# Kernel tuning notes

Hardware: AMD Instinct MI355X
Metric: run time of the kernel (lower is better)

Reference implementation:

```python
import jax, jax.numpy as jnp
import numpy as np

C_IN = 1024
C_MID = 512  # in_channels // shrink_factor


def conv1x1(x, w, b):
    # x: [B, Cin, H, W], w: [Cout, Cin], b: [Cout]
    return jnp.einsum('bchw,oc->bohw', x, w) + b[None, :, None, None]


def setup_inputs() -> dict:
    key = jax.random.key(0)
    ks = jax.random.split(key, 9)
    B, H, W = 8, 48, 48
    x = jax.random.normal(ks[0], (B, C_IN, H, W), dtype=jnp.float32)
    s = 0.02
    w1 = jax.random.normal(ks[1], (C_MID, C_IN), dtype=jnp.float32) * s
    b1 = jnp.zeros((C_MID,), dtype=jnp.float32)
    w2 = jax.random.normal(ks[2], (C_MID, C_IN), dtype=jnp.float32) * s
    b2 = jnp.zeros((C_MID,), dtype=jnp.float32)
    w3 = jax.random.normal(ks[3], (C_MID, C_IN), dtype=jnp.float32) * s
    b3 = jnp.zeros((C_MID,), dtype=jnp.float32)
    w4 = jax.random.normal(ks[4], (C_IN, C_MID), dtype=jnp.float32) * s
    b4 = jnp.zeros((C_IN,), dtype=jnp.float32)
    return {'x': x, 'w1': w1, 'b1': b1, 'w2': w2, 'b2': b2,
            'w3': w3, 'b3': b3, 'w4': w4, 'b4': b4}


def reference(x, w1, b1, w2, b2, w3, b3, w4, b4):
    B, C, H, W = x.shape
    # 1x1 conv projections (theta, phi, g), each [B, C_MID, H, W]
    x_theta = conv1x1(x, w1, b1)
    x_phi = conv1x1(x, w2, b2)
    x_g = conv1x1(x, w3, b3)
    # NOTE: the original uses raw .view() (no transpose); torch and jnp are both
    # row-major, so jnp.reshape reproduces the exact same memory reinterpretation.
    x_g = x_g.reshape(B, -1, C_MID)      # [B, N, C_MID]
    x_theta = x_theta.reshape(B, -1, C_MID)  # [B, N, C_MID]
    x_phi = x_phi.reshape(B, C_MID, -1)  # [B, C_MID, N]
    # full dense N x N affinity (N = H*W)
    att = jnp.einsum('bnc,bcm->bnm', x_theta, x_phi)
    att = jax.nn.softmax(att, axis=-1)
    y = jnp.einsum('bnm,bmc->bnc', att, x_g)  # [B, N, C_MID]
    y = y.reshape(B, C_MID, H, W)
    x_last = conv1x1(y, w4, b4)  # [B, C_IN, H, W]
    return x + x_last
```

## Files before the change

kernel.cpp:

```cpp
#include <hip/hip_runtime.h>

typedef unsigned short u16;
typedef __bf16 bf16x8_t __attribute__((ext_vector_type(8)));
typedef float f32x4_t __attribute__((ext_vector_type(4)));

__device__ __forceinline__ u16 f2bf(float f) {
  unsigned u = __builtin_bit_cast(unsigned, f);
  u += 0x7FFFu + ((u >> 16) & 1u);
  return (u16)(u >> 16);
}
__device__ __forceinline__ float bf2f(u16 h) {
  unsigned u = ((unsigned)h) << 16;
  return __builtin_bit_cast(float, u);
}

typedef __attribute__((address_space(1))) const unsigned gas_u32;
typedef __attribute__((address_space(3))) unsigned las_u32;
__device__ __forceinline__ void gload16(const void* g, void* l) {
  __builtin_amdgcn_global_load_lds((gas_u32*)g, (las_u32*)l, 16, 0, 0);
}

#define SBAR()                                  \
  do {                                          \
    __builtin_amdgcn_sched_barrier(0);          \
    asm volatile("" ::: "memory");              \
    __builtin_amdgcn_s_barrier();               \
    asm volatile("" ::: "memory");              \
    __builtin_amdgcn_sched_barrier(0);          \
  } while (0)
#define VM4() asm volatile("s_waitcnt vmcnt(4)" ::: "memory")

__global__ __launch_bounds__(256) void cast4_kernel(
    const float* __restrict__ a0, const float* __restrict__ a1,
    const float* __restrict__ a2, const float* __restrict__ a3,
    u16* __restrict__ out) {
  const int z = blockIdx.z;
  const float* a = (z == 0) ? a0 : (z == 1) ? a1 : (z == 2) ? a2 : a3;
  const int i = blockIdx.x * 256 + threadIdx.x;
  out[(size_t)z * 524288 + i] = f2bf(a[i]);
}

__global__ __launch_bounds__(256) void bcat_kernel(
    const float* __restrict__ b1, const float* __restrict__ b3,
    float* __restrict__ o) {
  const int i = blockIdx.x * 256 + threadIdx.x;
  o[i] = (i < 512) ? b1[i] : b3[i - 512];
}

__global__ __launch_bounds__(256) void cast_transpose_kernel(
    const float* __restrict__ in, u16* __restrict__ out, int R, int C,
    long sIn, long sOut) {
  __shared__ u16 t[32][33];
  const int b = blockIdx.z;
  in += (long)b * sIn;
  out += (long)b * sOut;
  const int c0 = blockIdx.x * 32, r0 = blockIdx.y * 32;
  const int tx = threadIdx.x, ty = threadIdx.y;
#pragma unroll
  for (int i = 0; i < 32; i += 8)
    t[ty + i][tx] = f2bf(in[(long)(r0 + ty + i) * C + c0 + tx]);
  __syncthreads();
#pragma unroll
  for (int i = 0; i < 32; i += 8)
    out[(long)(c0 + ty + i) * R + r0 + tx] = t[tx][ty + i];
}

__global__ __launch_bounds__(256) void transpose64(
    const u16* __restrict__ in, u16* __restrict__ out, int R, int C, long sIn,
    long sOut) {
  __shared__ u16 t[64][66];
  const int b = blockIdx.z;
  in += (long)b * sIn;
  out += (long)b * sOut;
  const int c0 = blockIdx.x * 64, r0 = blockIdx.y * 64;
  const int tx = threadIdx.x & 31, ty = threadIdx.x >> 5;
#pragma unroll
  for (int i = 0; i < 64; i += 8) {
    unsigned v = *(const unsigned*)&in[(long)(r0 + ty + i) * C + c0 + 2 * tx];
    t[ty + i][2 * tx] = (u16)v;
    t[ty + i][2 * tx + 1] = (u16)(v >> 16);
  }
  __syncthreads();
#pragma unroll
  for (int i = 0; i < 64; i += 8) {
    unsigned lo = t[2 * tx][ty + i], hi = t[2 * tx + 1][ty + i];
    *(unsigned*)&out[(long)(c0 + ty + i) * R + r0 + 2 * tx] = lo | (hi << 16);
  }
}

#define STG_A(bufv, h, kt)                                          \
  do {                                                              \
    const char* g_ = Ag + (size_t)(kt) * 128 + (size_t)(h)*AH;      \
    char* d_ = sAd + (bufv)*32768 + (h)*16384;                      \
    gload16(g_, d_);                                                \
    gload16(g_ + AC, d_ + 8192);                                    \
  } while (0)
#define STG_B(bufv, h, kt)                                          \
  do {                                                              \
    const char* g_ = Bg + (size_t)(kt) * 128 + (size_t)(h)*BH;      \
    char* d_ = sBd + (bufv)*32768 + (h)*16384;                      \
    gload16(g_, d_);                                                \
    gload16(g_ + BC, d_ + 8192);                                    \
  } while (0)
#define LOAD_A(bufv, mh)                                                     \
  _Pragma("unroll") for (int m = 0; m < 4; m++) {                            \
    const int lr_ = (mh)*128 + wr * 64 + m * 16 + l15;                       \
    af[m][0] = *(const bf16x8_t*)(lds + (bufv)*32768 + lr_ * 128 + koff0);   \
    af[m][1] =                                                               \
        *(const bf16x8_t*)(lds + (bufv)*32768 + lr_ * 128 + (koff0 ^ 64));   \
  }
#define LOAD_B(bufv, nh)                                                     \
  _Pragma("unroll") for (int n = 0; n < 2; n++) {                            \
    const int lr_ = (nh)*128 + wc * 32 + n * 16 + l15;                       \
    bfr[(nh)*2 + n][0] =                                                     \
        *(const bf16x8_t*)(lds + 65536 + (bufv)*32768 + lr_ * 128 + koff0);  \
    bfr[(nh)*2 + n][1] = *(const bf16x8_t*)(lds + 65536 + (bufv)*32768 +     \
                                            lr_ * 128 + (koff0 ^ 64));       \
  }
#define MMA(mh, nh)                                                          \
  __builtin_amdgcn_s_setprio(1);                                            \
  _Pragma("unroll") for (int m = 0; m < 4; m++)                              \
      _Pragma("unroll") for (int n = 0; n < 2; n++)                          \
          _Pragma("unroll") for (int kk = 0; kk < 2; kk++)                   \
              acc[(mh)*4 + m][(nh)*2 + n] =                                  \
      __builtin_amdgcn_mfma_f32_16x16x32_bf16(                               \
          af[m][kk], bfr[(nh)*2 + n][kk], acc[(mh)*4 + m][(nh)*2 + n], 0, 0, \
          0);                                                                \
  __builtin_amdgcn_s_setprio(0);

template <int MODE>
__global__ __launch_bounds__(512, 2) void gemm8(
    const u16* __restrict__ A, const u16* __restrict__ B,
    void* __restrict__ C0, void* __restrict__ C1, void* __restrict__ C2,
    const u16* __restrict__ W2, const float* __restrict__ bias,
    const float* __restrict__ bias2, const float* __restrict__ resid,
    float* __restrict__ stats) {
  constexpr int LDA_ = (MODE == 0) ? 1024 : (MODE == 3) ? 2304 : 512;
  constexpr int LDB_ = (MODE == 0) ? 1024 : (MODE == 3) ? 2304 : 512;
  constexpr int KK = (MODE == 0) ? 1024 : (MODE == 3) ? 2304 : 512;
  constexpr int NT = KK >> 6;
  constexpr size_t AH = 64ull * LDA_ * 2, AC = 128ull * LDA_ * 2;
  constexpr size_t BH = 32ull * LDB_ * 2, BC = 128ull * LDB_ * 2;

  __shared__ alignas(16) char lds[131072];
  const int tid = threadIdx.x;
  const int w = tid >> 6, l = tid & 63;
  const int wr = w >> 2, wc = w & 3;
  const int l15 = l & 15, lhi = l >> 4;
  const int koff0 = (lhi * 16) ^ ((l & 7) << 4);

  unsigned bx, by, bz;
  bool roleB = false;
  if constexpr (MODE == 0) {
    unsigned bid = blockIdx.x;
    unsigned swz = (bid & 7u) * 54u + (bid >> 3);
    roleB = (swz >= 288u);
    unsigned s = roleB ? swz - 288u : swz;
    if (roleB) { bx = s % 2u; by = (s / 2u) % 9u; bz = s / 18u; }
    else       { bx = s % 9u; by = (s / 9u) % 4u; bz = s / 36u; }
  } else {
    const unsigned gx = gridDim.x, gy = gridDim.y;
    const unsigned nb = gx * gy * gridDim.z;
    unsigned bid = blockIdx.x + gx * (blockIdx.y + gy * blockIdx.z);
    bid = (bid & 7u) * (nb >> 3) + (bid >> 3);
    bx = bid % gx;
    unsigned t1 = bid / gx;
    by = t1 % gy;
    bz = t1 / gy;
  }
  const int rowbase = by * 256, colbase = bx * 256;

  const u16* Abase;
  const u16* Bbase;
  if constexpr (MODE == 0) {
    Abase = roleB ? (B + (size_t)bz * 2359296) : A;
    Bbase = roleB ? W2 : (B + (size_t)bz * 2359296);
  } else if constexpr (MODE == 1) {
    Abase = A + (size_t)bz * 1179648;
    Bbase = B + (size_t)bz * 1179648;
  } else if constexpr (MODE == 3) {
    Abase = A + (size_t)bz * 5308416;
    Bbase = B + (size_t)bz * 1179648;
  } else {
    Abase = A;
    Bbase = B + (size_t)bz * 1179648;
  }

  const int sub = tid >> 3;
  const int kb = ((tid & 7) * 16) ^ ((sub & 7) << 4);
  const char* Ag = (const char*)(Abase + (size_t)(rowbase + sub) * LDA_) + kb;
  const char* Bg =
      (const char*)(Bbase + (size_t)(colbase + (sub >> 5) * 64 + (sub & 31)) *
                                LDB_) +
      kb;
  char* sAd = lds + w * 1024;
  char* sBd = lds + 65536 + w * 1024;

  f32x4_t acc[8][4] = {};
  bf16x8_t af[4][2], bfr[4][2];

  STG_A(0, 0, 0); STG_B(0, 0, 0);
  STG_A(0, 1, 0); STG_B(0, 1, 0);
  STG_A(1, 0, 1); STG_B(1, 0, 1);
  VM4();
  SBAR();

  for (int t = 0; t < NT; ++t) {
    const int c = t & 1;
    const int tn = (t + 1 < NT) ? t + 1 : NT - 1;
    const int tn2 = (t + 2 < NT) ? t + 2 : NT - 1;
    LOAD_A(c, 0);
    LOAD_B(c, 0);
    STG_A(c ^ 1, 1, tn);
    SBAR();
    MMA(0, 0);
    SBAR();
    LOAD_B(c, 1);
    STG_B(c ^ 1, 1, tn);
    SBAR();
    MMA(0, 1);
    SBAR();
    LOAD_A(c, 1);
    STG_A(c, 0, tn2);
    SBAR();
    MMA(1, 0);
    SBAR();
    STG_B(c, 0, tn2);
    VM4();
    SBAR();
    MMA(1, 1);
    SBAR();
  }

  if constexpr (MODE == 0) {
    if (!roleB) {
      const int rb = rowbase + wr * 128;
      const int which = rb >> 9;
      u16* Cp = (u16*)(which ? C1 : C0) + (size_t)bz * 1179648;
      const int rowout0 = rb - which * 512;
#pragma unroll
      for (int mf = 0; mf < 8; mf++)
#pragma unroll
        for (int r = 0; r < 4; r++) {
          const int ro = mf * 16 + lhi * 4 + r;
          const float bv = bias[rb + ro];
          const size_t rowo = (size_t)(rowout0 + ro) * 2304;
#pragma unroll
          for (int nf = 0; nf < 4; nf++) {
            const int col = colbase + wc * 64 + nf * 16 + l15;
            Cp[rowo + col] = f2bf(acc[mf][nf][r] + bv);
          }
        }
    } else {
      u16* Cp = (u16*)C2 + (size_t)bz * 1179648;
#pragma unroll
      for (int mf = 0; mf < 8; mf++)
#pragma unroll
        for (int r = 0; r < 4; r++) {
          const size_t rowo =
              (size_t)(rowbase + wr * 128 + mf * 16 + lhi * 4 + r) * 512;
#pragma unroll
          for (int nf = 0; nf < 4; nf++) {
            const int col = colbase + wc * 64 + nf * 16 + l15;
            Cp[rowo + col] = f2bf(acc[mf][nf][r] + bias2[col]);
          }
        }
    }
  } else if constexpr (MODE == 1) {
    u16* Cp = (u16*)C0 + (size_t)bz * 5308416;
#pragma unroll
    for (int mf = 0; mf < 8; mf++)
#pragma unroll
      for (int r = 0; r < 4; r++) {
        const int row = rowbase + wr * 128 + mf * 16 + lhi * 4 + r;
        float sm = 0.f;
#pragma unroll
        for (int nf = 0; nf < 4; nf++) {
          const int col = colbase + wc * 64 + nf * 16 + l15;
          const u16 hb = f2bf(__expf(acc[mf][nf][r]));
          Cp[(size_t)row * 2304 + col] = hb;
          sm += bf2f(hb);
        }
#pragma unroll
        for (int mk = 1; mk < 16; mk <<= 1) sm += __shfl_xor(sm, mk);
        if (l15 == 0)
          stats[((size_t)bz * 36 + bx * 4 + wc) * 2304 + row] = sm;
      }
  } else if constexpr (MODE == 3) {
    u16* Cp = (u16*)C0 + (size_t)bz * 1179648;
#pragma unroll
    for (int mf = 0; mf < 8; mf++)
#pragma unroll
      for (int r = 0; r < 4; r++) {
        const int row = rowbase + wr * 128 + mf * 16 + lhi * 4 + r;
        const float invs = stats[(size_t)bz * 2304 + row];
#pragma unroll
        for (int nf = 0; nf < 4; nf++) {
          const int col = colbase + wc * 64 + nf * 16 + l15;
          Cp[(size_t)row * 512 + col] = f2bf(acc[mf][nf][r] * invs);
        }
      }
  } else {
    float* Cp = (float*)C0 + (size_t)bz * 2359296;
    const float* rp = resid + (size_t)bz * 2359296;
#pragma unroll
    for (int mf = 0; mf < 8; mf++)
#pragma unroll
      for (int r = 0; r < 4; r++) {
        const int row = rowbase + wr * 128 + mf * 16 + lhi * 4 + r;
        const float bv = bias[row];
#pragma unroll
        for (int nf = 0; nf < 4; nf++) {
          const int col = colbase + wc * 64 + nf * 16 + l15;
          Cp[(size_t)row * 2304 + col] =
              acc[mf][nf][r] + bv + rp[(size_t)row * 2304 + col];
        }
      }
  }
}

__global__ __launch_bounds__(256) void reduce_sums(
    const float* __restrict__ stats, float* __restrict__ rowinv) {
  const int i = blockIdx.x * 256 + threadIdx.x;
  const int bz = i / 2304, n = i % 2304;
  const float* s = stats + (size_t)bz * 36 * 2304 + n;
  float S = 0.f;
  for (int j = 0; j < 36; j++) S += s[(size_t)j * 2304];
  rowinv[i] = 1.0f / S;
}

extern "C" void kernel_launch(void* const* d_in, const int* in_sizes, int n_in,
                              void* d_out, int out_size, void* d_ws,
                              size_t ws_size, hipStream_t stream) {
  const float* x = (const float*)d_in[0];
  const float* w1 = (const float*)d_in[1];
  const float* b1 = (const float*)d_in[2];
  const float* w2 = (const float*)d_in[3];
  const float* b2 = (const float*)d_in[4];
  const float* w3 = (const float*)d_in[5];
  const float* b3 = (const float*)d_in[6];
  const float* w4 = (const float*)d_in[7];
  const float* b4 = (const float*)d_in[8];
  float* out = (float*)d_out;
  char* ws = (char*)d_ws;

  if (ws_size < 268435456ull) return;
  u16* p_xT = (u16*)(ws);
  u16* p_gn = (u16*)(ws + 37748736);
  float* p_bcat = (float*)(ws + 56623104);
  u16* p_att = (u16*)(ws);
  float* p_stats = (float*)(ws + 84934656);
  float* p_rinv = (float*)(ws + 87588864);
  u16* p_wb = (u16*)(ws + 169869312);
  u16* p_theta = (u16*)(ws + 174063616);
  u16* p_phiT = (u16*)(ws + 192937984);
  u16* p_gT = (u16*)(ws + 211812352);
  u16* p_y = (u16*)(ws + 230686720);
  u16* p_yrT = (u16*)(ws + 249561088);

  cast4_kernel<<<dim3(2048, 1, 4), 256, 0, stream>>>(w1, w3, w2, w4, p_wb);
  bcat_kernel<<<dim3(4), 256, 0, stream>>>(b1, b3, p_bcat);
  cast_transpose_kernel<<<dim3(72, 32, 8), dim3(32, 8), 0, stream>>>(
      x, p_xT, 1024, 2304, 2359296L, 2359296L);
  gemm8<0><<<dim3(432), 512, 0, stream>>>(
      p_wb, p_xT, p_theta, p_gn, p_phiT, p_wb + 1048576, p_bcat, b2, nullptr,
      nullptr);
  transpose64<<<dim3(8, 36, 8), 256, 0, stream>>>(p_gn, p_gT, 2304, 512,
                                                  1179648L, 1179648L);
  gemm8<1><<<dim3(9, 9, 8), 512, 0, stream>>>(
      p_theta, p_phiT, p_att, nullptr, nullptr, nullptr, nullptr, nullptr,
      nullptr, p_stats);
  reduce_sums<<<dim3(72), 256, 0, stream>>>(p_stats, p_rinv);
  gemm8<3><<<dim3(2, 9, 8), 512, 0, stream>>>(
      p_att, p_gT, p_y, nullptr, nullptr, nullptr, nullptr, nullptr, nullptr,
      p_rinv);
  transpose64<<<dim3(36, 8, 8), 256, 0, stream>>>(p_y, p_yrT, 512, 2304,
                                                  1179648L, 1179648L);
  gemm8<2><<<dim3(9, 4, 8), 512, 0, stream>>>(
      p_wb + 1572864, p_yrT, out, nullptr, nullptr, nullptr, b4, nullptr, x,
      nullptr);
}
```

Measured before the change: 308.7 us.

## Fuse attention score, exp, and PV GEMMs into one flash-style kernel

```diff
diff --git a/kernel.cpp b/kernel.cpp
--- a/kernel.cpp
+++ b/kernel.cpp
@@ -28,7 +28,11 @@
     asm volatile("" ::: "memory");              \
     __builtin_amdgcn_sched_barrier(0);          \
   } while (0)
+#define VM0() asm volatile("s_waitcnt vmcnt(0)" ::: "memory")
+#define VM2() asm volatile("s_waitcnt vmcnt(2)" ::: "memory")
 #define VM4() asm volatile("s_waitcnt vmcnt(4)" ::: "memory")
+#define VM8() asm volatile("s_waitcnt vmcnt(8)" ::: "memory")
+#define LGKM0() asm volatile("s_waitcnt lgkmcnt(0)" ::: "memory")
 
 __global__ __launch_bounds__(256) void cast4_kernel(
     const float* __restrict__ a0, const float* __restrict__ a1,
@@ -133,11 +137,10 @@
     const u16* __restrict__ A, const u16* __restrict__ B,
     void* __restrict__ C0, void* __restrict__ C1, void* __restrict__ C2,
     const u16* __restrict__ W2, const float* __restrict__ bias,
-    const float* __restrict__ bias2, const float* __restrict__ resid,
-    float* __restrict__ stats) {
-  constexpr int LDA_ = (MODE == 0) ? 1024 : (MODE == 3) ? 2304 : 512;
-  constexpr int LDB_ = (MODE == 0) ? 1024 : (MODE == 3) ? 2304 : 512;
-  constexpr int KK = (MODE == 0) ? 1024 : (MODE == 3) ? 2304 : 512;
+    const float* __restrict__ bias2, const float* __restrict__ resid) {
+  constexpr int LDA_ = (MODE == 0) ? 1024 : 512;
+  constexpr int LDB_ = (MODE == 0) ? 1024 : 512;
+  constexpr int KK = (MODE == 0) ? 1024 : 512;
   constexpr int NT = KK >> 6;
   constexpr size_t AH = 64ull * LDA_ * 2, AC = 128ull * LDA_ * 2;
   constexpr size_t BH = 32ull * LDB_ * 2, BC = 128ull * LDB_ * 2;
@@ -175,12 +178,6 @@
   if constexpr (MODE == 0) {
     Abase = roleB ? (B + (size_t)bz * 2359296) : A;
     Bbase = roleB ? W2 : (B + (size_t)bz * 2359296);
-  } else if constexpr (MODE == 1) {
-    Abase = A + (size_t)bz * 1179648;
-    Bbase = B + (size_t)bz * 1179648;
-  } else if constexpr (MODE == 3) {
-    Abase = A + (size_t)bz * 5308416;
-    Bbase = B + (size_t)bz * 1179648;
   } else {
     Abase = A;
     Bbase = B + (size_t)bz * 1179648;
@@ -266,40 +263,6 @@
           }
         }
     }
-  } else if constexpr (MODE == 1) {
-    u16* Cp = (u16*)C0 + (size_t)bz * 5308416;
-#pragma unroll
-    for (int mf = 0; mf < 8; mf++)
-#pragma unroll
-      for (int r = 0; r < 4; r++) {
-        const int row = rowbase + wr * 128 + mf * 16 + lhi * 4 + r;
-        float sm = 0.f;
-#pragma unroll
-        for (int nf = 0; nf < 4; nf++) {
-          const int col = colbase + wc * 64 + nf * 16 + l15;
-          const u16 hb = f2bf(__expf(acc[mf][nf][r]));
-          Cp[(size_t)row * 2304 + col] = hb;
-          sm += bf2f(hb);
-        }
-#pragma unroll
-        for (int mk = 1; mk < 16; mk <<= 1) sm += __shfl_xor(sm, mk);
-        if (l15 == 0)
-          stats[((size_t)bz * 36 + bx * 4 + wc) * 2304 + row] = sm;
-      }
-  } else if constexpr (MODE == 3) {
-    u16* Cp = (u16*)C0 + (size_t)bz * 1179648;
-#pragma unroll
-    for (int mf = 0; mf < 8; mf++)
-#pragma unroll
-      for (int r = 0; r < 4; r++) {
-        const int row = rowbase + wr * 128 + mf * 16 + lhi * 4 + r;
-        const float invs = stats[(size_t)bz * 2304 + row];
-#pragma unroll
-        for (int nf = 0; nf < 4; nf++) {
-          const int col = colbase + wc * 64 + nf * 16 + l15;
-          Cp[(size_t)row * 512 + col] = f2bf(acc[mf][nf][r] * invs);
-        }
-      }
   } else {
     float* Cp = (float*)C0 + (size_t)bz * 2359296;
     const float* rp = resid + (size_t)bz * 2359296;
@@ -319,14 +282,181 @@
   }
 }
 
-__global__ __launch_bounds__(256) void reduce_sums(
-    const float* __restrict__ stats, float* __restrict__ rowinv) {
-  const int i = blockIdx.x * 256 + threadIdx.x;
-  const int bz = i / 2304, n = i % 2304;
-  const float* s = stats + (size_t)bz * 36 * 2304 + n;
-  float S = 0.f;
-  for (int j = 0; j < 36; j++) S += s[(size_t)j * 2304];
-  rowinv[i] = 1.0f / S;
+__global__ __launch_bounds__(512, 1) void fused_attn(
+    const u16* __restrict__ TH, const u16* __restrict__ PHI,
+    const u16* __restrict__ GT, u16* __restrict__ Y) {
+  __shared__ alignas(16) char lds[163840];
+  const int tid = threadIdx.x;
+  const int w = tid >> 6, l = tid & 63;
+  const int l15 = l & 15, lhi = l >> 4;
+  const int koff0 = (lhi * 16) ^ ((l & 7) << 4);
+  const int wr = w >> 2, wcS = w & 3;
+  const int nloc = wcS * 16 + l15;
+
+  unsigned bid = blockIdx.x;
+  bid = (bid & 7u) * 36u + (bid >> 3);
+  const unsigned bz = bid / 36u, iq = bid % 36u;
+  const int n0 = iq * 64;
+
+  const int sub = tid >> 3;
+  const int kb = ((tid & 7) * 16) ^ ((sub & 7) << 4);
+
+  const char* THb =
+      (const char*)(TH + (size_t)bz * 1179648 + (size_t)(n0 + sub) * 512) + kb;
+  const char* PHb0 =
+      (const char*)(PHI + (size_t)bz * 1179648 + (size_t)sub * 512) + kb;
+  const char* GTb0 =
+      (const char*)(GT + (size_t)bz * 1179648 + (size_t)sub * 2304) + kb;
+  u16* Yb = Y + (size_t)bz * 1179648;
+  float* rsf = (float*)(lds + 65536);
+
+  f32x4_t yacc[4][4] = {};
+  float pr = 0.f;
+  bf16x8_t af[4][2], bfr[4][2], bt[2];
+
+#define S_STG_A(bufv, h, kt)                                           \
+  do {                                                                 \
+    const char* g_ = PHm + (size_t)(kt)*128 + (size_t)(h)*65536;       \
+    char* d_ = lds + (bufv)*32768 + (h)*16384 + w * 1024;              \
+    gload16(g_, d_);                                                   \
+    gload16(g_ + 131072, d_ + 8192);                                   \
+  } while (0)
+#define S_STG_T(bufv, kt)                                              \
+  gload16(THb + (size_t)(kt)*128, lds + 65536 + (bufv)*8192 + w * 1024)
+#define S_LOAD_A(bufv, mh)                                                   \
+  _Pragma("unroll") for (int m = 0; m < 4; m++) {                            \
+    const int lr_ = (mh)*128 + wr * 64 + m * 16 + l15;                       \
+    af[m][0] = *(const bf16x8_t*)(lds + (bufv)*32768 + lr_ * 128 + koff0);   \
+    af[m][1] =                                                               \
+        *(const bf16x8_t*)(lds + (bufv)*32768 + lr_ * 128 + (koff0 ^ 64));   \
+  }
+#define S_LOAD_T(bufv)                                                       \
+  do {                                                                       \
+    const int lr_ = wcS * 16 + l15;                                          \
+    bt[0] =                                                                  \
+        *(const bf16x8_t*)(lds + 65536 + (bufv)*8192 + lr_ * 128 + koff0);   \
+    bt[1] = *(const bf16x8_t*)(lds + 65536 + (bufv)*8192 + lr_ * 128 +       \
+                               (koff0 ^ 64));                                \
+  } while (0)
+#define S_MMA(mh)                                                            \
+  __builtin_amdgcn_s_setprio(1);                                            \
+  _Pragma("unroll") for (int m = 0; m < 4; m++)                              \
+      _Pragma("unroll") for (int kk = 0; kk < 2; kk++)                       \
+          sacc[(mh)*4 + m] = __builtin_amdgcn_mfma_f32_16x16x32_bf16(        \
+              af[m][kk], bt[kk], sacc[(mh)*4 + m], 0, 0, 0);                 \
+  __builtin_amdgcn_s_setprio(0);
+#define PV_STG_G(bufv, ks)                                                   \
+  _Pragma("unroll") for (int q = 0; q < 8; q++)                              \
+      gload16(GTm + (size_t)q * 294912 + (size_t)(ks)*128,                   \
+              lds + (bufv)*65536 + q * 8192 + w * 1024);
+#define PV_LOAD_A(ks)                                                        \
+  _Pragma("unroll") for (int m = 0; m < 4; m++) {                            \
+    const int br_ = m * 16 + l15;                                            \
+    af[m][0] = *(const bf16x8_t*)(lds + 131072 + br_ * 512 +                 \
+                                  (((ks)*128 + lhi * 16) ^                   \
+                                   ((l15 & 7) << 4)));                       \
+    af[m][1] = *(const bf16x8_t*)(lds + 131072 + br_ * 512 +                 \
+                                  (((ks)*128 + 64 + lhi * 16) ^              \
+                                   ((l15 & 7) << 4)));                       \
+  }
+#define PV_LOAD_G(bufv)                                                      \
+  _Pragma("unroll") for (int n = 0; n < 4; n++) {                            \
+    const int lr_ = w * 64 + n * 16 + l15;                                   \
+    bfr[n][0] = *(const bf16x8_t*)(lds + (bufv)*65536 + lr_ * 128 + koff0);  \
+    bfr[n][1] =                                                              \
+        *(const bf16x8_t*)(lds + (bufv)*65536 + lr_ * 128 + (koff0 ^ 64));   \
+  }
+#define PV_MMA()                                                             \
+  __builtin_amdgcn_s_setprio(1);                                            \
+  _Pragma("unroll") for (int m = 0; m < 4; m++)                              \
+      _Pragma("unroll") for (int n = 0; n < 4; n++)                          \
+          _Pragma("unroll") for (int kk = 0; kk < 2; kk++)                   \
+              yacc[m][n] = __builtin_amdgcn_mfma_f32_16x16x32_bf16(          \
+                  af[m][kk], bfr[n][kk], yacc[m][n], 0, 0, 0);               \
+  __builtin_amdgcn_s_setprio(0);
+
+  for (int mt = 0; mt < 9; ++mt) {
+    const char* PHm = PHb0 + (size_t)mt * 262144;
+    const char* GTm = GTb0 + (size_t)mt * 512;
+
+    f32x4_t sacc[8] = {};
+    S_STG_A(0, 0, 0); S_STG_A(0, 1, 0); S_STG_T(0, 0);
+    S_STG_A(1, 0, 1);
+    VM2();
+    SBAR();
+    for (int t = 0; t < 8; ++t) {
+      const int c = t & 1;
+      const int tn = (t + 1 < 8) ? t + 1 : 7;
+      const int tn2 = (t + 2 < 8) ? t + 2 : 7;
+      S_LOAD_A(c, 0);
+      S_LOAD_T(c);
+      S_STG_A(c ^ 1, 1, tn);
+      S_STG_T(c ^ 1, tn);
+      SBAR();
+      S_MMA(0);
+      SBAR();
+      S_LOAD_A(c, 1);
+      S_STG_A(c, 0, tn2);
+      SBAR();
+      S_MMA(1);
+      VM2();
+      SBAR();
+    }
+
+#pragma unroll
+    for (int mf = 0; mf < 8; mf++)
+#pragma unroll
+      for (int r = 0; r < 4; r++) {
+        const int mm = wr * 128 + (mf >> 2) * 64 + (mf & 3) * 16 + lhi * 4 + r;
+        const u16 hb = f2bf(__expf(sacc[mf][r]));
+        pr += bf2f(hb);
+        *(u16*)(lds + 131072 + nloc * 512 +
+                ((2 * mm) ^ ((nloc & 7) << 4))) = hb;
+      }
+    VM0();
+    LGKM0();
+    SBAR();
+
+    PV_STG_G(0, 0);
+    for (int ks = 0; ks < 4; ++ks) {
+      const int c = ks & 1;
+      if (ks < 3) {
+        PV_STG_G(c ^ 1, ks + 1);
+        VM8();
+      } else {
+        VM0();
+      }
+      SBAR();
+      PV_LOAD_A(ks);
+      PV_LOAD_G(c);
+      PV_MMA();
+      SBAR();
+    }
+  }
+
+  SBAR();
+  if (tid < 64) rsf[tid] = 0.f;
+  LGKM0();
+  SBAR();
+  float prs = pr;
+  prs += __shfl_xor(prs, 16);
+  prs += __shfl_xor(prs, 32);
+  if (lhi == 0) atomicAdd(&rsf[nloc], prs);
+  LGKM0();
+  SBAR();
+#pragma unroll
+  for (int mf = 0; mf < 4; mf++)
+#pragma unroll
+    for (int r = 0; r < 4; r++) {
+      const int n = mf * 16 + lhi * 4 + r;
+      const float inv = 1.0f / rsf[n];
+      const size_t rowo = (size_t)(n0 + n) * 512;
+#pragma unroll
+      for (int nf = 0; nf < 4; nf++) {
+        const int d = w * 64 + nf * 16 + l15;
+        Yb[rowo + d] = f2bf(yacc[mf][nf][r] * inv);
+      }
+    }
 }
 
 extern "C" void kernel_launch(void* const* d_in, const int* in_sizes, int n_in,
@@ -348,9 +478,6 @@
   u16* p_xT = (u16*)(ws);
   u16* p_gn = (u16*)(ws + 37748736);
   float* p_bcat = (float*)(ws + 56623104);
-  u16* p_att = (u16*)(ws);
-  float* p_stats = (float*)(ws + 84934656);
-  float* p_rinv = (float*)(ws + 87588864);
   u16* p_wb = (u16*)(ws + 169869312);
   u16* p_theta = (u16*)(ws + 174063616);
   u16* p_phiT = (u16*)(ws + 192937984);
@@ -363,20 +490,12 @@
   cast_transpose_kernel<<<dim3(72, 32, 8), dim3(32, 8), 0, stream>>>(
       x, p_xT, 1024, 2304, 2359296L, 2359296L);
   gemm8<0><<<dim3(432), 512, 0, stream>>>(
-      p_wb, p_xT, p_theta, p_gn, p_phiT, p_wb + 1048576, p_bcat, b2, nullptr,
-      nullptr);
+      p_wb, p_xT, p_theta, p_gn, p_phiT, p_wb + 1048576, p_bcat, b2, nullptr);
   transpose64<<<dim3(8, 36, 8), 256, 0, stream>>>(p_gn, p_gT, 2304, 512,
                                                   1179648L, 1179648L);
-  gemm8<1><<<dim3(9, 9, 8), 512, 0, stream>>>(
-      p_theta, p_phiT, p_att, nullptr, nullptr, nullptr, nullptr, nullptr,
-      nullptr, p_stats);
-  reduce_sums<<<dim3(72), 256, 0, stream>>>(p_stats, p_rinv);
-  gemm8<3><<<dim3(2, 9, 8), 512, 0, stream>>>(
-      p_att, p_gT, p_y, nullptr, nullptr, nullptr, nullptr, nullptr, nullptr,
-      p_rinv);
+  fused_attn<<<dim3(288), 512, 0, stream>>>(p_theta, p_phiT, p_gT, p_y);
   transpose64<<<dim3(36, 8, 8), 256, 0, stream>>>(p_y, p_yrT, 512, 2304,
                                                   1179648L, 1179648L);
   gemm8<2><<<dim3(9, 4, 8), 512, 0, stream>>>(
-      p_wb + 1572864, p_yrT, out, nullptr, nullptr, nullptr, b4, nullptr, x,
-      nullptr);
-}
+      p_wb + 1572864, p_yrT, out, nullptr, nullptr, nullptr, b4, nullptr, x);
+}
```

Result: slower. 366.5 us (+18.7%).

## Replace PV GEMM with dedicated 256x128-tile kernel for better CU occupancy

Applied to the files above, without the earlier changes.

```diff
diff --git a/kernel.cpp b/kernel.cpp
--- a/kernel.cpp
+++ b/kernel.cpp
@@ -28,6 +28,7 @@
     asm volatile("" ::: "memory");              \
     __builtin_amdgcn_sched_barrier(0);          \
   } while (0)
+#define VM2() asm volatile("s_waitcnt vmcnt(2)" ::: "memory")
 #define VM4() asm volatile("s_waitcnt vmcnt(4)" ::: "memory")
 
 __global__ __launch_bounds__(256) void cast4_kernel(
@@ -135,9 +136,9 @@
     const u16* __restrict__ W2, const float* __restrict__ bias,
     const float* __restrict__ bias2, const float* __restrict__ resid,
     float* __restrict__ stats) {
-  constexpr int LDA_ = (MODE == 0) ? 1024 : (MODE == 3) ? 2304 : 512;
-  constexpr int LDB_ = (MODE == 0) ? 1024 : (MODE == 3) ? 2304 : 512;
-  constexpr int KK = (MODE == 0) ? 1024 : (MODE == 3) ? 2304 : 512;
+  constexpr int LDA_ = (MODE == 0) ? 1024 : 512;
+  constexpr int LDB_ = (MODE == 0) ? 1024 : 512;
+  constexpr int KK = (MODE == 0) ? 1024 : 512;
   constexpr int NT = KK >> 6;
   constexpr size_t AH = 64ull * LDA_ * 2, AC = 128ull * LDA_ * 2;
   constexpr size_t BH = 32ull * LDB_ * 2, BC = 128ull * LDB_ * 2;
@@ -178,9 +179,6 @@
   } else if constexpr (MODE == 1) {
     Abase = A + (size_t)bz * 1179648;
     Bbase = B + (size_t)bz * 1179648;
-  } else if constexpr (MODE == 3) {
-    Abase = A + (size_t)bz * 5308416;
-    Bbase = B + (size_t)bz * 1179648;
   } else {
     Abase = A;
     Bbase = B + (size_t)bz * 1179648;
@@ -286,20 +284,6 @@
         if (l15 == 0)
           stats[((size_t)bz * 36 + bx * 4 + wc) * 2304 + row] = sm;
       }
-  } else if constexpr (MODE == 3) {
-    u16* Cp = (u16*)C0 + (size_t)bz * 1179648;
-#pragma unroll
-    for (int mf = 0; mf < 8; mf++)
-#pragma unroll
-      for (int r = 0; r < 4; r++) {
-        const int row = rowbase + wr * 128 + mf * 16 + lhi * 4 + r;
-        const float invs = stats[(size_t)bz * 2304 + row];
-#pragma unroll
-        for (int nf = 0; nf < 4; nf++) {
-          const int col = colbase + wc * 64 + nf * 16 + l15;
-          Cp[(size_t)row * 512 + col] = f2bf(acc[mf][nf][r] * invs);
-        }
-      }
   } else {
     float* Cp = (float*)C0 + (size_t)bz * 2359296;
     const float* rp = resid + (size_t)bz * 2359296;
@@ -327,6 +311,120 @@
   float S = 0.f;
   for (int j = 0; j < 36; j++) S += s[(size_t)j * 2304];
   rowinv[i] = 1.0f / S;
+}
+
+__global__ __launch_bounds__(512, 1) void pv128(
+    const u16* __restrict__ A, const u16* __restrict__ B, u16* __restrict__ C,
+    const float* __restrict__ rowinv) {
+  constexpr int NT = 36;
+  constexpr size_t AH = 64ull * 2304 * 2, AC = 128ull * 2304 * 2;
+  constexpr size_t BHp = 64ull * 2304 * 2;
+
+  __shared__ alignas(16) char lds[98304];
+  const int tid = threadIdx.x;
+  const int w = tid >> 6, l = tid & 63;
+  const int wr = w >> 2, wc = w & 3;
+  const int l15 = l & 15, lhi = l >> 4;
+  const int koff0 = (lhi * 16) ^ ((l & 7) << 4);
+
+  const unsigned swz = (blockIdx.x & 7u) * 36u + (blockIdx.x >> 3);
+  const unsigned bz = swz / 36u, rem = swz % 36u;
+  const unsigned by = rem >> 2, bx = rem & 3u;
+  const int rowbase = by * 256, colbase = bx * 128;
+
+  const int sub = tid >> 3;
+  const int kb = ((tid & 7) * 16) ^ ((sub & 7) << 4);
+  const char* Ag =
+      (const char*)(A + (size_t)bz * 5308416 + (size_t)(rowbase + sub) * 2304) +
+      kb;
+  const char* Bg =
+      (const char*)(B + (size_t)bz * 1179648 + (size_t)(colbase + sub) * 2304) +
+      kb;
+  char* sAd = lds + w * 1024;
+
+#define PSTG_A(bufv, h, kt)                                          \
+  do {                                                               \
+    const char* g_ = Ag + (size_t)(kt) * 128 + (size_t)(h)*AH;       \
+    char* d_ = sAd + (bufv)*32768 + (h)*16384;                       \
+    gload16(g_, d_);                                                 \
+    gload16(g_ + AC, d_ + 8192);                                     \
+  } while (0)
+#define PSTG_B(bufv, h, kt)                                          \
+  gload16(Bg + (size_t)(kt) * 128 + (size_t)(h)*BHp,                 \
+          lds + 65536 + (bufv)*16384 + (h)*8192 + w * 1024)
+#define PLOAD_A(bufv, mh)                                                    \
+  _Pragma("unroll") for (int m = 0; m < 4; m++) {                            \
+    const int lr_ = (mh)*128 + wr * 64 + m * 16 + l15;                       \
+    af[m][0] = *(const bf16x8_t*)(lds + (bufv)*32768 + lr_ * 128 + koff0);   \
+    af[m][1] =                                                               \
+        *(const bf16x8_t*)(lds + (bufv)*32768 + lr_ * 128 + (koff0 ^ 64));   \
+  }
+#define PLOAD_B(bufv)                                                        \
+  _Pragma("unroll") for (int n = 0; n < 2; n++) {                            \
+    const int cc_ = wc * 32 + n * 16 + l15;                                  \
+    const int base_ = 65536 + (bufv)*16384 + (wc >> 1) * 8192 +              \
+                      (cc_ & 63) * 128;                                      \
+    bfr[n][0] = *(const bf16x8_t*)(lds + base_ + koff0);                     \
+    bfr[n][1] = *(const bf16x8_t*)(lds + base_ + (koff0 ^ 64));              \
+  }
+#define PMMA(mh)                                                             \
+  __builtin_amdgcn_s_setprio(1);                                            \
+  _Pragma("unroll") for (int m = 0; m < 4; m++)                              \
+      _Pragma("unroll") for (int n = 0; n < 2; n++)                          \
+          _Pragma("unroll") for (int kk = 0; kk < 2; kk++)                   \
+              acc[(mh)*4 + m][n] = __builtin_amdgcn_mfma_f32_16x16x32_bf16(  \
+                  af[m][kk], bfr[n][kk], acc[(mh)*4 + m][n], 0, 0, 0);       \
+  __builtin_amdgcn_s_setprio(0);
+
+  f32x4_t acc[8][2] = {};
+  bf16x8_t af[4][2], bfr[2][2];
+
+  PSTG_A(0, 0, 0);
+  PSTG_A(0, 1, 0);
+  PSTG_B(0, 0, 0);
+  PSTG_B(0, 1, 0);
+  PSTG_A(1, 0, 1);
+  VM2();
+  SBAR();
+
+  for (int t = 0; t < NT; ++t) {
+    const int c = t & 1;
+    const int tn = (t + 1 < NT) ? t + 1 : NT - 1;
+    const int tn2 = (t + 2 < NT) ? t + 2 : NT - 1;
+    PLOAD_A(c, 0);
+    PLOAD_B(c);
+    PSTG_A(c ^ 1, 1, tn);
+    PSTG_B(c ^ 1, 0, tn);
+    PSTG_B(c ^ 1, 1, tn);
+    SBAR();
+    PMMA(0);
+    SBAR();
+    PLOAD_A(c, 1);
+    PSTG_A(c, 0, tn2);
+    VM2();
+    SBAR();
+    PMMA(1);
+    SBAR();
+  }
+
+  const size_t cb = (size_t)bz * 1179648;
+#pragma unroll
+  for (int mf = 0; mf < 8; mf++)
+#pragma unroll
+    for (int r = 0; r < 4; r++) {
+      const int row = rowbase + wr * 128 + mf * 16 + lhi * 4 + r;
+      const float invs = rowinv[(size_t)bz * 2304 + row];
+#pragma unroll
+      for (int nf = 0; nf < 2; nf++) {
+        const int col = colbase + wc * 32 + nf * 16 + l15;
+        C[cb + (size_t)row * 512 + col] = f2bf(acc[mf][nf][r] * invs);
+      }
+    }
+#undef PSTG_A
+#undef PSTG_B
+#undef PLOAD_A
+#undef PLOAD_B
+#undef PMMA
 }
 
 extern "C" void kernel_launch(void* const* d_in, const int* in_sizes, int n_in,
@@ -371,9 +469,7 @@
       p_theta, p_phiT, p_att, nullptr, nullptr, nullptr, nullptr, nullptr,
       nullptr, p_stats);
   reduce_sums<<<dim3(72), 256, 0, stream>>>(p_stats, p_rinv);
-  gemm8<3><<<dim3(2, 9, 8), 512, 0, stream>>>(
-      p_att, p_gT, p_y, nullptr, nullptr, nullptr, nullptr, nullptr, nullptr,
-      p_rinv);
+  pv128<<<dim3(288), 512, 0, stream>>>(p_att, p_gT, p_y, p_rinv);
   transpose64<<<dim3(36, 8, 8), 256, 0, stream>>>(p_y, p_yrT, 512, 2304,
                                                   1179648L, 1179648L);
   gemm8<2><<<dim3(9, 4, 8), 512, 0, stream>>>(
```

Result: slower. 325.5 us (+5.4%).
